# Kernel optimization log

Hardware: AMD Instinct MI355X
Metric: run time of the kernel (lower is better)

## Reference

```python
import jax, jax.numpy as jnp
import numpy as np

D_MODEL = 1024
HEADS = 16
D_K = D_MODEL // HEADS
B, S = 2, 2048


def setup_inputs() -> dict:
    key = jax.random.key(0)
    ks = jax.random.split(key, 11)
    sc = 1.0 / np.sqrt(D_MODEL)
    return {
        "q": jax.random.normal(ks[0], (B, S, D_MODEL), jnp.float32),
        "k": jax.random.normal(ks[1], (B, S, D_MODEL), jnp.float32),
        "v": jax.random.normal(ks[2], (B, S, D_MODEL), jnp.float32),
        "Wq": jax.random.normal(ks[3], (D_MODEL, D_MODEL), jnp.float32) * sc,
        "bq": jnp.zeros((D_MODEL,), jnp.float32),
        "Wk": jax.random.normal(ks[4], (D_MODEL, D_MODEL), jnp.float32) * sc,
        "bk": jnp.zeros((D_MODEL,), jnp.float32),
        "Wv": jax.random.normal(ks[5], (D_MODEL, D_MODEL), jnp.float32) * sc,
        "bv": jnp.zeros((D_MODEL,), jnp.float32),
        "Wo": jax.random.normal(ks[6], (D_MODEL, D_MODEL), jnp.float32) * sc,
        "bo": jnp.zeros((D_MODEL,), jnp.float32),
    }


def reference(q, k, v, Wq, bq, Wk, bk, Wv, bv, Wo, bo):
    bs = q.shape[0]
    # linear projections then split heads: [B,S,D] -> [B,H,S,Dk]
    def proj(x, W, b):
        y = x @ W.T + b
        return y.reshape(bs, -1, HEADS, D_K).transpose(0, 2, 1, 3)

    qh = proj(q, Wq, bq)
    kh = proj(k, Wk, bk)
    vh = proj(v, Wv, bv)
    # scores: [B,H,Sq,Sk] -- full attention matrix as in the original
    scores = jnp.einsum("bhqd,bhkd->bhqk", qh, kh) / jnp.sqrt(
        jnp.asarray(D_K, jnp.float32))
    attn = jax.nn.softmax(scores, axis=-1)
    # dropout is identity in eval/reference mode
    out = jnp.einsum("bhqk,bhkd->bhqd", attn, vh)
    concat = out.transpose(0, 2, 1, 3).reshape(bs, -1, D_MODEL)
    return concat @ Wo.T + bo
```

## Files before the change

kernel.cpp:

```cpp
#include <hip/hip_runtime.h>
#include <hip/hip_bf16.h>

typedef __attribute__((ext_vector_type(8))) short bf16x8;
typedef __attribute__((ext_vector_type(4))) float f32x4;
typedef __attribute__((ext_vector_type(16))) float f32x16;

#define DM   1024
#define SEQ  2048
#define NB   2
#define NH   16
#define MR   (NB*SEQ)

#define SMK  (MR*DM)
#define W1M  (DM*DM)

#define QSCALE 0.18033688011112042f

#define OFF_QB  ((size_t)0)
#define OFF_KB  ((size_t)SMK)
#define OFF_VB  ((size_t)(2*(size_t)SMK))
#define OFF_WQ  ((size_t)(3*(size_t)SMK))
#define OFF_WO  ((size_t)(3*(size_t)SMK + 3*(size_t)W1M))
#define OFF_QP  ((size_t)(3*(size_t)SMK + 4*(size_t)W1M))
#define OFF_KP  ((size_t)(4*(size_t)SMK + 4*(size_t)W1M))
#define OFF_VP  ((size_t)(5*(size_t)SMK + 4*(size_t)W1M))
#define OFF_CC  ((size_t)0)

__device__ __forceinline__ unsigned short f2bf(float f) {
  union { __hip_bfloat16 b; unsigned short u; } cv;
  cv.b = __float2bfloat16(f);
  return cv.u;
}

__device__ __forceinline__ unsigned int cvtpk_bf16(float lo, float hi) {
  unsigned int r;
  asm("v_cvt_pk_bf16_f32 %0, %1, %2" : "=v"(r) : "v"(lo), "v"(hi));
  return r;
}

__device__ __forceinline__ void plane32_swap(unsigned int& a, unsigned int& b) {
  asm("v_permlane32_swap_b32 %0, %1" : "+v"(a), "+v"(b));
}

__global__ __launch_bounds__(256) void cvt_inputs(const float* __restrict__ q,
                                                  const float* __restrict__ k,
                                                  const float* __restrict__ v,
                                                  unsigned short* __restrict__ dst) {
  const int z = blockIdx.y;
  const float* src = (z == 0) ? q : ((z == 1) ? k : v);
  int i = blockIdx.x * 256 + threadIdx.x;
  float4 val = reinterpret_cast<const float4*>(src)[i];
  ushort4 o;
  o.x = f2bf(val.x); o.y = f2bf(val.y); o.z = f2bf(val.z); o.w = f2bf(val.w);
  reinterpret_cast<ushort4*>(dst + (size_t)z * SMK)[i] = o;
}

__global__ __launch_bounds__(256) void cvt_weights(const float* __restrict__ wq,
                                                   const float* __restrict__ wk,
                                                   const float* __restrict__ wv,
                                                   const float* __restrict__ wo,
                                                   unsigned short* __restrict__ dst) {
  const int z = blockIdx.y;
  const float* src = (z == 0) ? wq : ((z == 1) ? wk : ((z == 2) ? wv : wo));
  int i = blockIdx.x * 256 + threadIdx.x;
  float4 val = reinterpret_cast<const float4*>(src)[i];
  ushort4 o;
  o.x = f2bf(val.x); o.y = f2bf(val.y); o.z = f2bf(val.z); o.w = f2bf(val.w);
  reinterpret_cast<ushort4*>(dst + (size_t)z * W1M)[i] = o;
}

__device__ __forceinline__ void gload_lds16(const void* g, void* l) {
  __builtin_amdgcn_global_load_lds(
      (const __attribute__((address_space(1))) unsigned int*)g,
      (__attribute__((address_space(3))) unsigned int*)l,
      16, 0, 0);
}

template<int BM, int BN, bool OUT_BF16, bool BIAS_ROW>
__device__ __forceinline__ void gemm_bt_body(unsigned short* __restrict__ As,
                                             unsigned short* __restrict__ Bs,
                                             const unsigned short* __restrict__ A,
                                             const unsigned short* __restrict__ Bt,
                                             const float* __restrict__ bias,
                                             void* __restrict__ Cv,
                                             int N, int K, float scale,
                                             int brow, int bcol) {
  constexpr int MREP = BM / 32;
  constexpr int NREP = BN / 32;
  const int tid  = threadIdx.x;
  const int lane = tid & 63;
  const int w    = tid >> 6;
  const int wr   = w >> 1, wc = w & 1;

  f32x4 acc[MREP][NREP];
#pragma unroll
  for (int m = 0; m < MREP; m++)
#pragma unroll
    for (int n = 0; n < NREP; n++) acc[m][n] = (f32x4){0.f, 0.f, 0.f, 0.f};

  const int srow = lane >> 2;
  const int scol = (lane & 3) * 8;

  auto stage = [&](int buf, int k0) {
#pragma unroll
    for (int c = w; c < BM / 16; c += 4)
      gload_lds16(A + (size_t)(brow + c * 16 + srow) * K + k0 + scol,
                  (char*)As + (size_t)buf * BM * 64 + c * 1024);
#pragma unroll
    for (int c = w; c < BN / 16; c += 4)
      gload_lds16(Bt + (size_t)(bcol + c * 16 + srow) * K + k0 + scol,
                  (char*)Bs + (size_t)buf * BN * 64 + c * 1024);
  };

  stage(0, 0);
  __syncthreads();

  const int nk = K / 32;
  const int lrow_a = wr * (BM / 2) + (lane & 15);
  const int lrow_b = wc * (BN / 2) + (lane & 15);
  const int lcol   = (lane >> 4) * 8;

  for (int kt = 0; kt < nk; ++kt) {
    int buf = kt & 1;
    if (kt + 1 < nk) stage(buf ^ 1, (kt + 1) * 32);
    bf16x8 a[MREP], b[NREP];
#pragma unroll
    for (int m = 0; m < MREP; m++)
      a[m] = *(const bf16x8*)&As[(size_t)buf * BM * 32 + (lrow_a + m * 16) * 32 + lcol];
#pragma unroll
    for (int n = 0; n < NREP; n++)
      b[n] = *(const bf16x8*)&Bs[(size_t)buf * BN * 32 + (lrow_b + n * 16) * 32 + lcol];
    __builtin_amdgcn_s_setprio(1);
#pragma unroll
    for (int m = 0; m < MREP; m++)
#pragma unroll
      for (int n = 0; n < NREP; n++)
        acc[m][n] = __builtin_amdgcn_mfma_f32_16x16x32_bf16(a[m], b[n], acc[m][n], 0, 0, 0);
    __builtin_amdgcn_s_setprio(0);
    __syncthreads();
  }

  const int crow0 = brow + wr * (BM / 2);
  const int ccol0 = bcol + wc * (BN / 2);
  const int rsub  = (lane >> 4) * 4;
  const int csub  = lane & 15;
#pragma unroll
  for (int m = 0; m < MREP; m++)
#pragma unroll
    for (int n = 0; n < NREP; n++) {
      int col = ccol0 + n * 16 + csub;
      float bcol_v = BIAS_ROW ? 0.f : bias[col];
#pragma unroll
      for (int q = 0; q < 4; q++) {
        int row = crow0 + m * 16 + rsub + q;
        float bb = BIAS_ROW ? bias[row] : bcol_v;
        float v = (acc[m][n][q] + bb) * scale;
        if (OUT_BF16)
          ((unsigned short*)Cv)[(size_t)row * N + col] = f2bf(v);
        else
          ((float*)Cv)[(size_t)row * N + col] = v;
      }
    }
}

__global__ __launch_bounds__(256) void gemm_qkv(unsigned short* ws,
                                                const float* __restrict__ bq,
                                                const float* __restrict__ bk,
                                                const float* __restrict__ bv) {
  __shared__ unsigned short As[2 * 128 * 32];
  __shared__ unsigned short Bs[2 * 128 * 32];
  const int z = blockIdx.z;
  const int bid = blockIdx.x;
  if (z < 2) {
    int bx = bid & 7, by = bid >> 3;
    gemm_bt_body<128, 128, true, false>(
        As, Bs,
        ws + OFF_QB + (size_t)z * SMK, ws + OFF_WQ + (size_t)z * W1M,
        z ? bk : bq, ws + OFF_QP + (size_t)z * SMK,
        DM, DM, z ? 1.f : QSCALE, by * 128, bx * 128);
  } else {
    int bx = bid & 31, by = bid >> 5;
    gemm_bt_body<128, 128, true, true>(
        As, Bs,
        ws + OFF_WQ + 2 * W1M, ws + OFF_VB,
        bv, ws + OFF_VP,
        MR, DM, 1.f, by * 128, bx * 128);
  }
}

__global__ __launch_bounds__(256) void gemm_out(const unsigned short* __restrict__ ws,
                                                const float* __restrict__ bo,
                                                float* __restrict__ out) {
  __shared__ unsigned short As[2 * 64 * 32];
  __shared__ unsigned short Bs[2 * 128 * 32];
  gemm_bt_body<64, 128, false, false>(
      As, Bs,
      ws + OFF_CC, ws + OFF_WO, bo, out,
      DM, DM, 1.f, blockIdx.y * 64, blockIdx.x * 128);
}

__global__ __launch_bounds__(512, 4) void flash_attn(unsigned short* ws) {
  __shared__ __align__(16) unsigned char smem[65536];

  const int tid  = threadIdx.x;
  const int lane = tid & 63;
  const int w    = tid >> 6;
  const int s    = w >> 2;
  const int wsub = w & 3;
  const int q    = lane & 31;
  const int hi   = lane >> 5;
  const int swq  = q & 7;
  const int bid  = blockIdx.x;
  const int swzb = (bid & 7) * 64 + (bid >> 3);
  const int qblk = swzb & 15;
  const int bh   = swzb >> 4;
  const int b    = bh >> 4, h = bh & 15;

  const unsigned short* Qp = ws + OFF_QP;
  const unsigned short* Kp = ws + OFF_KP;
  const unsigned short* Vp = ws + OFF_VP;
  unsigned short* CC = ws + OFF_CC;

  const unsigned short* Kg = Kp + (size_t)(b * SEQ) * DM + h * 64;
  const unsigned short* Vg = Vp + (size_t)(h * 64) * MR + (size_t)b * SEQ;

  bf16x8 bqf[4];
  {
    const unsigned short* qrow =
        Qp + (size_t)(b * SEQ + qblk * 128 + wsub * 32 + q) * DM + h * 64;
#pragma unroll
    for (int c = 0; c < 4; c++)
      bqf[c] = *(const bf16x8*)(qrow + c * 16 + hi * 8);
  }

  f32x16 o_acc[2];
#pragma unroll
  for (int dt = 0; dt < 2; dt++)
#pragma unroll
    for (int r = 0; r < 16; r++) o_acc[dt][r] = 0.f;
  float l_run = 0.f;

  auto stage = [&](int buf, int t) {
    const unsigned short* Kt = Kg + (size_t)(s * 16 + t) * 64 * DM;
    const unsigned short* Vt = Vg + (s * 16 + t) * 64;
    char* base = (char*)smem + (size_t)(s * 2 + buf) * 16384;
#pragma unroll
    for (int i = 0; i < 2; i++) {
      int slot = wsub * 128 + i * 64 + lane;
      int srow = slot >> 3;
      int gch  = (slot & 7) ^ (srow & 7);
      gload_lds16(Kt + (size_t)srow * DM + gch * 8, base + slot * 16);
      gload_lds16(Vt + (size_t)srow * MR + gch * 8, base + 8192 + slot * 16);
    }
  };

  stage(0, 0);

  for (int t = 0; t < 16; ++t) {
    int buf = t & 1;
    __syncthreads();
    if (t + 1 < 16) stage(buf ^ 1, t + 1);
    const unsigned short* Kb = (const unsigned short*)(smem + (size_t)(s * 2 + buf) * 16384);
    const unsigned short* Vb = Kb + 4096;

    f32x16 st0, st1;
#pragma unroll
    for (int r = 0; r < 16; r++) { st0[r] = 0.f; st1[r] = 0.f; }
    __builtin_amdgcn_s_setprio(1);
#pragma unroll
    for (int c = 0; c < 4; c++) {
      int ch = (((c << 1) | hi) ^ swq) << 3;
      bf16x8 ak0 = *(const bf16x8*)&Kb[q * 64 + ch];
      bf16x8 ak1 = *(const bf16x8*)&Kb[(32 + q) * 64 + ch];
      st0 = __builtin_amdgcn_mfma_f32_32x32x16_bf16(ak0, bqf[c], st0, 0, 0, 0);
      st1 = __builtin_amdgcn_mfma_f32_32x32x16_bf16(ak1, bqf[c], st1, 0, 0, 0);
    }
    __builtin_amdgcn_s_setprio(0);

    unsigned int pk0[8], pk1[8];
    float lt = 0.f;
#pragma unroll
    for (int p = 0; p < 8; p++) {
      float a0 = __builtin_amdgcn_exp2f(st0[2 * p]);
      float a1 = __builtin_amdgcn_exp2f(st0[2 * p + 1]);
      float b0 = __builtin_amdgcn_exp2f(st1[2 * p]);
      float b1 = __builtin_amdgcn_exp2f(st1[2 * p + 1]);
      lt += (a0 + a1) + (b0 + b1);
      pk0[p] = cvtpk_bf16(a0, a1);
      pk1[p] = cvtpk_bf16(b0, b1);
    }
    l_run += lt;

    plane32_swap(pk0[0], pk0[2]); plane32_swap(pk0[1], pk0[3]);
    plane32_swap(pk0[4], pk0[6]); plane32_swap(pk0[5], pk0[7]);
    plane32_swap(pk1[0], pk1[2]); plane32_swap(pk1[1], pk1[3]);
    plane32_swap(pk1[4], pk1[6]); plane32_swap(pk1[5], pk1[7]);

    __builtin_amdgcn_s_setprio(1);
#pragma unroll
    for (int t4 = 0; t4 < 4; t4++) {
      union { unsigned int u[4]; bf16x8 v; } pb;
      const unsigned int* src = (t4 < 2) ? pk0 : pk1;
      pb.u[0] = src[(t4 & 1) * 4 + 0];
      pb.u[1] = src[(t4 & 1) * 4 + 1];
      pb.u[2] = src[(t4 & 1) * 4 + 2];
      pb.u[3] = src[(t4 & 1) * 4 + 3];
      int ch = (((t4 << 1) | hi) ^ swq) << 3;
#pragma unroll
      for (int dt = 0; dt < 2; dt++) {
        bf16x8 av = *(const bf16x8*)&Vb[(dt * 32 + q) * 64 + ch];
        o_acc[dt] = __builtin_amdgcn_mfma_f32_32x32x16_bf16(av, pb.v, o_acc[dt], 0, 0, 0);
      }
    }
    __builtin_amdgcn_s_setprio(0);
  }

  __syncthreads();
  float* scr = (float*)smem;
  float lsum = l_run + __shfl_xor(l_run, 32, 64);
  if (s == 1) {
    int idx = (wsub * 64 + lane) * 33;
#pragma unroll
    for (int dt = 0; dt < 2; dt++)
#pragma unroll
      for (int r = 0; r < 16; r++) scr[idx + dt * 16 + r] = o_acc[dt][r];
    scr[idx + 32] = lsum;
  }
  __syncthreads();
  if (s == 0) {
    int idx = (wsub * 64 + lane) * 33;
#pragma unroll
    for (int dt = 0; dt < 2; dt++)
#pragma unroll
      for (int r = 0; r < 16; r++) o_acc[dt][r] += scr[idx + dt * 16 + r];
    float l = lsum + scr[idx + 32];
    float inv = 1.f / l;

    int qg = b * SEQ + qblk * 128 + wsub * 32 + q;
    unsigned short* crow = CC + (size_t)qg * DM + h * 64;
#pragma unroll
    for (int dt = 0; dt < 2; dt++)
#pragma unroll
      for (int rq = 0; rq < 4; rq++) {
        ushort4 o;
        o.x = f2bf(o_acc[dt][4 * rq + 0] * inv);
        o.y = f2bf(o_acc[dt][4 * rq + 1] * inv);
        o.z = f2bf(o_acc[dt][4 * rq + 2] * inv);
        o.w = f2bf(o_acc[dt][4 * rq + 3] * inv);
        *(ushort4*)&crow[dt * 32 + rq * 8 + hi * 4] = o;
      }
  }
}

extern "C" void kernel_launch(void* const* d_in, const int* in_sizes, int n_in,
                              void* d_out, int out_size, void* d_ws, size_t ws_size,
                              hipStream_t stream) {
  const float* q  = (const float*)d_in[0];
  const float* k  = (const float*)d_in[1];
  const float* v  = (const float*)d_in[2];
  const float* Wq = (const float*)d_in[3];
  const float* bq = (const float*)d_in[4];
  const float* Wk = (const float*)d_in[5];
  const float* bk = (const float*)d_in[6];
  const float* Wv = (const float*)d_in[7];
  const float* bv = (const float*)d_in[8];
  const float* Wo = (const float*)d_in[9];
  const float* bo = (const float*)d_in[10];

  unsigned short* ws = (unsigned short*)d_ws;
  float* out = (float*)d_out;

  cvt_inputs<<<dim3(SMK / 1024, 3), dim3(256), 0, stream>>>(q, k, v, ws + OFF_QB);
  cvt_weights<<<dim3(W1M / 1024, 4), dim3(256), 0, stream>>>(Wq, Wk, Wv, Wo, ws + OFF_WQ);

  gemm_qkv<<<dim3(256, 1, 3), dim3(256), 0, stream>>>(ws, bq, bk, bv);

  flash_attn<<<dim3(512), dim3(512), 0, stream>>>(ws);

  gemm_out<<<dim3(DM / 128, MR / 64, 1), dim3(256), 0, stream>>>(ws, bo, out);
}
```

Before: 126.0 us.

## Triple-buffer GEMM and attention loads, double query rows per attention block

```diff
diff --git a/kernel.cpp b/kernel.cpp
--- a/kernel.cpp
+++ b/kernel.cpp
@@ -87,6 +87,7 @@
                                              int brow, int bcol) {
   constexpr int MREP = BM / 32;
   constexpr int NREP = BN / 32;
+  constexpr int LPS  = BM / 64 + BN / 64;
   const int tid  = threadIdx.x;
   const int lane = tid & 63;
   const int w    = tid >> 6;
@@ -113,23 +114,34 @@
   };
 
   stage(0, 0);
-  __syncthreads();
+  stage(1, 32);
 
   const int nk = K / 32;
   const int lrow_a = wr * (BM / 2) + (lane & 15);
   const int lrow_b = wc * (BN / 2) + (lane & 15);
   const int lcol   = (lane >> 4) * 8;
 
+  int b0 = 0;
   for (int kt = 0; kt < nk; ++kt) {
-    int buf = kt & 1;
-    if (kt + 1 < nk) stage(buf ^ 1, (kt + 1) * 32);
+    if (kt + 1 < nk) {
+      if constexpr (LPS == 4) asm volatile("s_waitcnt vmcnt(4)" ::: "memory");
+      else                    asm volatile("s_waitcnt vmcnt(3)" ::: "memory");
+    } else {
+      asm volatile("s_waitcnt vmcnt(0)" ::: "memory");
+    }
+    __builtin_amdgcn_s_barrier();
+    __builtin_amdgcn_sched_barrier(0);
+    if (kt + 2 < nk) {
+      int bn = b0 + 2; if (bn >= 3) bn -= 3;
+      stage(bn, (kt + 2) * 32);
+    }
     bf16x8 a[MREP], b[NREP];
 #pragma unroll
     for (int m = 0; m < MREP; m++)
-      a[m] = *(const bf16x8*)&As[(size_t)buf * BM * 32 + (lrow_a + m * 16) * 32 + lcol];
+      a[m] = *(const bf16x8*)&As[(size_t)b0 * BM * 32 + (lrow_a + m * 16) * 32 + lcol];
 #pragma unroll
     for (int n = 0; n < NREP; n++)
-      b[n] = *(const bf16x8*)&Bs[(size_t)buf * BN * 32 + (lrow_b + n * 16) * 32 + lcol];
+      b[n] = *(const bf16x8*)&Bs[(size_t)b0 * BN * 32 + (lrow_b + n * 16) * 32 + lcol];
     __builtin_amdgcn_s_setprio(1);
 #pragma unroll
     for (int m = 0; m < MREP; m++)
@@ -137,7 +149,7 @@
       for (int n = 0; n < NREP; n++)
         acc[m][n] = __builtin_amdgcn_mfma_f32_16x16x32_bf16(a[m], b[n], acc[m][n], 0, 0, 0);
     __builtin_amdgcn_s_setprio(0);
-    __syncthreads();
+    b0 = (b0 == 2) ? 0 : b0 + 1;
   }
 
   const int crow0 = brow + wr * (BM / 2);
@@ -151,10 +163,10 @@
       int col = ccol0 + n * 16 + csub;
       float bcol_v = BIAS_ROW ? 0.f : bias[col];
 #pragma unroll
-      for (int q = 0; q < 4; q++) {
-        int row = crow0 + m * 16 + rsub + q;
+      for (int qq = 0; qq < 4; qq++) {
+        int row = crow0 + m * 16 + rsub + qq;
         float bb = BIAS_ROW ? bias[row] : bcol_v;
-        float v = (acc[m][n][q] + bb) * scale;
+        float v = (acc[m][n][qq] + bb) * scale;
         if (OUT_BF16)
           ((unsigned short*)Cv)[(size_t)row * N + col] = f2bf(v);
         else
@@ -167,8 +179,8 @@
                                                 const float* __restrict__ bq,
                                                 const float* __restrict__ bk,
                                                 const float* __restrict__ bv) {
-  __shared__ unsigned short As[2 * 128 * 32];
-  __shared__ unsigned short Bs[2 * 128 * 32];
+  __shared__ unsigned short As[3 * 128 * 32];
+  __shared__ unsigned short Bs[3 * 128 * 32];
   const int z = blockIdx.z;
   const int bid = blockIdx.x;
   if (z < 2) {
@@ -191,16 +203,16 @@
 __global__ __launch_bounds__(256) void gemm_out(const unsigned short* __restrict__ ws,
                                                 const float* __restrict__ bo,
                                                 float* __restrict__ out) {
-  __shared__ unsigned short As[2 * 64 * 32];
-  __shared__ unsigned short Bs[2 * 128 * 32];
+  __shared__ unsigned short As[3 * 64 * 32];
+  __shared__ unsigned short Bs[3 * 128 * 32];
   gemm_bt_body<64, 128, false, false>(
       As, Bs,
       ws + OFF_CC, ws + OFF_WO, bo, out,
       DM, DM, 1.f, blockIdx.y * 64, blockIdx.x * 128);
 }
 
-__global__ __launch_bounds__(512, 4) void flash_attn(unsigned short* ws) {
-  __shared__ __align__(16) unsigned char smem[65536];
+__global__ __launch_bounds__(512, 2) void flash_attn(unsigned short* ws) {
+  __shared__ __align__(16) unsigned char smem[98304];
 
   const int tid  = threadIdx.x;
   const int lane = tid & 63;
@@ -211,9 +223,9 @@
   const int hi   = lane >> 5;
   const int swq  = q & 7;
   const int bid  = blockIdx.x;
-  const int swzb = (bid & 7) * 64 + (bid >> 3);
-  const int qblk = swzb & 15;
-  const int bh   = swzb >> 4;
+  const int swzb = (bid & 7) * 32 + (bid >> 3);
+  const int qblk = swzb & 7;
+  const int bh   = swzb >> 3;
   const int b    = bh >> 4, h = bh & 15;
 
   const unsigned short* Qp = ws + OFF_QP;
@@ -224,26 +236,29 @@
   const unsigned short* Kg = Kp + (size_t)(b * SEQ) * DM + h * 64;
   const unsigned short* Vg = Vp + (size_t)(h * 64) * MR + (size_t)b * SEQ;
 
-  bf16x8 bqf[4];
-  {
+  bf16x8 bqf[2][4];
+#pragma unroll
+  for (int s2 = 0; s2 < 2; s2++) {
     const unsigned short* qrow =
-        Qp + (size_t)(b * SEQ + qblk * 128 + wsub * 32 + q) * DM + h * 64;
+        Qp + (size_t)(b * SEQ + qblk * 256 + wsub * 64 + s2 * 32 + q) * DM + h * 64;
 #pragma unroll
     for (int c = 0; c < 4; c++)
-      bqf[c] = *(const bf16x8*)(qrow + c * 16 + hi * 8);
-  }
-
-  f32x16 o_acc[2];
-#pragma unroll
-  for (int dt = 0; dt < 2; dt++)
-#pragma unroll
-    for (int r = 0; r < 16; r++) o_acc[dt][r] = 0.f;
-  float l_run = 0.f;
+      bqf[s2][c] = *(const bf16x8*)(qrow + c * 16 + hi * 8);
+  }
+
+  f32x16 o_acc[2][2];
+  float l_run[2] = {0.f, 0.f};
+#pragma unroll
+  for (int s2 = 0; s2 < 2; s2++)
+#pragma unroll
+    for (int dt = 0; dt < 2; dt++)
+#pragma unroll
+      for (int r = 0; r < 16; r++) o_acc[s2][dt][r] = 0.f;
 
   auto stage = [&](int buf, int t) {
     const unsigned short* Kt = Kg + (size_t)(s * 16 + t) * 64 * DM;
     const unsigned short* Vt = Vg + (s * 16 + t) * 64;
-    char* base = (char*)smem + (size_t)(s * 2 + buf) * 16384;
+    char* base = (char*)smem + (size_t)(s * 3 + buf) * 16384;
 #pragma unroll
     for (int i = 0; i < 2; i++) {
       int slot = wsub * 128 + i * 64 + lane;
@@ -255,100 +270,125 @@
   };
 
   stage(0, 0);
-
+  stage(1, 1);
+
+  int bcur = 0;
   for (int t = 0; t < 16; ++t) {
-    int buf = t & 1;
-    __syncthreads();
-    if (t + 1 < 16) stage(buf ^ 1, t + 1);
-    const unsigned short* Kb = (const unsigned short*)(smem + (size_t)(s * 2 + buf) * 16384);
+    if (t < 15) asm volatile("s_waitcnt vmcnt(4)" ::: "memory");
+    else        asm volatile("s_waitcnt vmcnt(0)" ::: "memory");
+    __builtin_amdgcn_s_barrier();
+    __builtin_amdgcn_sched_barrier(0);
+    if (t + 2 < 16) {
+      int bn = bcur + 2; if (bn >= 3) bn -= 3;
+      stage(bn, t + 2);
+    }
+    const unsigned short* Kb = (const unsigned short*)(smem + (size_t)(s * 3 + bcur) * 16384);
     const unsigned short* Vb = Kb + 4096;
 
-    f32x16 st0, st1;
-#pragma unroll
-    for (int r = 0; r < 16; r++) { st0[r] = 0.f; st1[r] = 0.f; }
+    f32x16 st[2][2];
+#pragma unroll
+    for (int s2 = 0; s2 < 2; s2++)
+#pragma unroll
+      for (int r = 0; r < 16; r++) { st[s2][0][r] = 0.f; st[s2][1][r] = 0.f; }
     __builtin_amdgcn_s_setprio(1);
 #pragma unroll
     for (int c = 0; c < 4; c++) {
       int ch = (((c << 1) | hi) ^ swq) << 3;
       bf16x8 ak0 = *(const bf16x8*)&Kb[q * 64 + ch];
       bf16x8 ak1 = *(const bf16x8*)&Kb[(32 + q) * 64 + ch];
-      st0 = __builtin_amdgcn_mfma_f32_32x32x16_bf16(ak0, bqf[c], st0, 0, 0, 0);
-      st1 = __builtin_amdgcn_mfma_f32_32x32x16_bf16(ak1, bqf[c], st1, 0, 0, 0);
+      st[0][0] = __builtin_amdgcn_mfma_f32_32x32x16_bf16(ak0, bqf[0][c], st[0][0], 0, 0, 0);
+      st[0][1] = __builtin_amdgcn_mfma_f32_32x32x16_bf16(ak1, bqf[0][c], st[0][1], 0, 0, 0);
+      st[1][0] = __builtin_amdgcn_mfma_f32_32x32x16_bf16(ak0, bqf[1][c], st[1][0], 0, 0, 0);
+      st[1][1] = __builtin_amdgcn_mfma_f32_32x32x16_bf16(ak1, bqf[1][c], st[1][1], 0, 0, 0);
     }
     __builtin_amdgcn_s_setprio(0);
 
-    unsigned int pk0[8], pk1[8];
-    float lt = 0.f;
-#pragma unroll
-    for (int p = 0; p < 8; p++) {
-      float a0 = __builtin_amdgcn_exp2f(st0[2 * p]);
-      float a1 = __builtin_amdgcn_exp2f(st0[2 * p + 1]);
-      float b0 = __builtin_amdgcn_exp2f(st1[2 * p]);
-      float b1 = __builtin_amdgcn_exp2f(st1[2 * p + 1]);
-      lt += (a0 + a1) + (b0 + b1);
-      pk0[p] = cvtpk_bf16(a0, a1);
-      pk1[p] = cvtpk_bf16(b0, b1);
-    }
-    l_run += lt;
-
-    plane32_swap(pk0[0], pk0[2]); plane32_swap(pk0[1], pk0[3]);
-    plane32_swap(pk0[4], pk0[6]); plane32_swap(pk0[5], pk0[7]);
-    plane32_swap(pk1[0], pk1[2]); plane32_swap(pk1[1], pk1[3]);
-    plane32_swap(pk1[4], pk1[6]); plane32_swap(pk1[5], pk1[7]);
+    unsigned int pk[2][2][8];
+#pragma unroll
+    for (int s2 = 0; s2 < 2; s2++) {
+      float lt = 0.f;
+#pragma unroll
+      for (int p = 0; p < 8; p++) {
+        float e0 = __builtin_amdgcn_exp2f(st[s2][0][2 * p]);
+        float e1 = __builtin_amdgcn_exp2f(st[s2][0][2 * p + 1]);
+        float e2 = __builtin_amdgcn_exp2f(st[s2][1][2 * p]);
+        float e3 = __builtin_amdgcn_exp2f(st[s2][1][2 * p + 1]);
+        lt += (e0 + e1) + (e2 + e3);
+        pk[s2][0][p] = cvtpk_bf16(e0, e1);
+        pk[s2][1][p] = cvtpk_bf16(e2, e3);
+      }
+      l_run[s2] += lt;
+      plane32_swap(pk[s2][0][0], pk[s2][0][2]); plane32_swap(pk[s2][0][1], pk[s2][0][3]);
+      plane32_swap(pk[s2][0][4], pk[s2][0][6]); plane32_swap(pk[s2][0][5], pk[s2][0][7]);
+      plane32_swap(pk[s2][1][0], pk[s2][1][2]); plane32_swap(pk[s2][1][1], pk[s2][1][3]);
+      plane32_swap(pk[s2][1][4], pk[s2][1][6]); plane32_swap(pk[s2][1][5], pk[s2][1][7]);
+    }
 
     __builtin_amdgcn_s_setprio(1);
 #pragma unroll
     for (int t4 = 0; t4 < 4; t4++) {
-      union { unsigned int u[4]; bf16x8 v; } pb;
-      const unsigned int* src = (t4 < 2) ? pk0 : pk1;
-      pb.u[0] = src[(t4 & 1) * 4 + 0];
-      pb.u[1] = src[(t4 & 1) * 4 + 1];
-      pb.u[2] = src[(t4 & 1) * 4 + 2];
-      pb.u[3] = src[(t4 & 1) * 4 + 3];
       int ch = (((t4 << 1) | hi) ^ swq) << 3;
+      union { unsigned int u[4]; bf16x8 v; } pb0, pb1;
+#pragma unroll
+      for (int j = 0; j < 4; j++) {
+        pb0.u[j] = pk[0][t4 >> 1][(t4 & 1) * 4 + j];
+        pb1.u[j] = pk[1][t4 >> 1][(t4 & 1) * 4 + j];
+      }
 #pragma unroll
       for (int dt = 0; dt < 2; dt++) {
         bf16x8 av = *(const bf16x8*)&Vb[(dt * 32 + q) * 64 + ch];
-        o_acc[dt] = __builtin_amdgcn_mfma_f32_32x32x16_bf16(av, pb.v, o_acc[dt], 0, 0, 0);
+        o_acc[0][dt] = __builtin_amdgcn_mfma_f32_32x32x16_bf16(av, pb0.v, o_acc[0][dt], 0, 0, 0);
+        o_acc[1][dt] = __builtin_amdgcn_mfma_f32_32x32x16_bf16(av, pb1.v, o_acc[1][dt], 0, 0, 0);
       }
     }
     __builtin_amdgcn_s_setprio(0);
+    bcur = (bcur == 2) ? 0 : bcur + 1;
   }
 
   __syncthreads();
   float* scr = (float*)smem;
-  float lsum = l_run + __shfl_xor(l_run, 32, 64);
+  float lsum[2];
+#pragma unroll
+  for (int s2 = 0; s2 < 2; s2++)
+    lsum[s2] = l_run[s2] + __shfl_xor(l_run[s2], 32, 64);
+  const int gi = wsub * 64 + lane;
   if (s == 1) {
-    int idx = (wsub * 64 + lane) * 33;
-#pragma unroll
-    for (int dt = 0; dt < 2; dt++)
-#pragma unroll
-      for (int r = 0; r < 16; r++) scr[idx + dt * 16 + r] = o_acc[dt][r];
-    scr[idx + 32] = lsum;
+#pragma unroll
+    for (int s2 = 0; s2 < 2; s2++) {
+#pragma unroll
+      for (int dt = 0; dt < 2; dt++)
+#pragma unroll
+        for (int r = 0; r < 16; r++)
+          scr[gi * 67 + s2 * 33 + dt * 16 + r] = o_acc[s2][dt][r];
+      scr[gi * 67 + s2 * 33 + 32] = lsum[s2];
+    }
   }
   __syncthreads();
   if (s == 0) {
-    int idx = (wsub * 64 + lane) * 33;
-#pragma unroll
-    for (int dt = 0; dt < 2; dt++)
-#pragma unroll
-      for (int r = 0; r < 16; r++) o_acc[dt][r] += scr[idx + dt * 16 + r];
-    float l = lsum + scr[idx + 32];
-    float inv = 1.f / l;
-
-    int qg = b * SEQ + qblk * 128 + wsub * 32 + q;
-    unsigned short* crow = CC + (size_t)qg * DM + h * 64;
-#pragma unroll
-    for (int dt = 0; dt < 2; dt++)
-#pragma unroll
-      for (int rq = 0; rq < 4; rq++) {
-        ushort4 o;
-        o.x = f2bf(o_acc[dt][4 * rq + 0] * inv);
-        o.y = f2bf(o_acc[dt][4 * rq + 1] * inv);
-        o.z = f2bf(o_acc[dt][4 * rq + 2] * inv);
-        o.w = f2bf(o_acc[dt][4 * rq + 3] * inv);
-        *(ushort4*)&crow[dt * 32 + rq * 8 + hi * 4] = o;
-      }
+#pragma unroll
+    for (int s2 = 0; s2 < 2; s2++) {
+#pragma unroll
+      for (int dt = 0; dt < 2; dt++)
+#pragma unroll
+        for (int r = 0; r < 16; r++)
+          o_acc[s2][dt][r] += scr[gi * 67 + s2 * 33 + dt * 16 + r];
+      float l = lsum[s2] + scr[gi * 67 + s2 * 33 + 32];
+      float inv = 1.f / l;
+
+      int qg = b * SEQ + qblk * 256 + wsub * 64 + s2 * 32 + q;
+      unsigned short* crow = CC + (size_t)qg * DM + h * 64;
+#pragma unroll
+      for (int dt = 0; dt < 2; dt++)
+#pragma unroll
+        for (int rq = 0; rq < 4; rq++) {
+          ushort4 o;
+          o.x = f2bf(o_acc[s2][dt][4 * rq + 0] * inv);
+          o.y = f2bf(o_acc[s2][dt][4 * rq + 1] * inv);
+          o.z = f2bf(o_acc[s2][dt][4 * rq + 2] * inv);
+          o.w = f2bf(o_acc[s2][dt][4 * rq + 3] * inv);
+          *(ushort4*)&crow[dt * 32 + rq * 8 + hi * 4] = o;
+        }
+    }
   }
 }
 
@@ -375,7 +415,7 @@
 
   gemm_qkv<<<dim3(256, 1, 3), dim3(256), 0, stream>>>(ws, bq, bk, bv);
 
-  flash_attn<<<dim3(512), dim3(512), 0, stream>>>(ws);
+  flash_attn<<<dim3(256), dim3(512), 0, stream>>>(ws);
 
   gemm_out<<<dim3(DM / 128, MR / 64, 1), dim3(256), 0, stream>>>(ws, bo, out);
 }
```

Result: faster. 120.9 us (-4.0%).

## Triple-buffer GEMM LDS staging with vmcnt waits and merge conversion kernels

Applied to the files above, without the earlier changes.

```diff
diff --git a/kernel.cpp b/kernel.cpp
--- a/kernel.cpp
+++ b/kernel.cpp
@@ -42,31 +42,34 @@
   asm("v_permlane32_swap_b32 %0, %1" : "+v"(a), "+v"(b));
 }
 
-__global__ __launch_bounds__(256) void cvt_inputs(const float* __restrict__ q,
-                                                  const float* __restrict__ k,
-                                                  const float* __restrict__ v,
-                                                  unsigned short* __restrict__ dst) {
-  const int z = blockIdx.y;
-  const float* src = (z == 0) ? q : ((z == 1) ? k : v);
+__global__ __launch_bounds__(256) void cvt_all(const float* __restrict__ q,
+                                               const float* __restrict__ k,
+                                               const float* __restrict__ v,
+                                               const float* __restrict__ wq,
+                                               const float* __restrict__ wk,
+                                               const float* __restrict__ wv,
+                                               const float* __restrict__ wo,
+                                               unsigned short* __restrict__ ws) {
   int i = blockIdx.x * 256 + threadIdx.x;
-  float4 val = reinterpret_cast<const float4*>(src)[i];
+  const float* src;
+  unsigned short* dst;
+  int j;
+  if (i < 3 * (SMK / 4)) {
+    int z = i >> 20;
+    j = i & ((SMK / 4) - 1);
+    src = (z == 0) ? q : ((z == 1) ? k : v);
+    dst = ws + OFF_QB + (size_t)z * SMK;
+  } else {
+    int i2 = i - 3 * (SMK / 4);
+    int z = i2 >> 18;
+    j = i2 & ((W1M / 4) - 1);
+    src = (z == 0) ? wq : ((z == 1) ? wk : ((z == 2) ? wv : wo));
+    dst = ws + OFF_WQ + (size_t)z * W1M;
+  }
+  float4 val = reinterpret_cast<const float4*>(src)[j];
   ushort4 o;
   o.x = f2bf(val.x); o.y = f2bf(val.y); o.z = f2bf(val.z); o.w = f2bf(val.w);
-  reinterpret_cast<ushort4*>(dst + (size_t)z * SMK)[i] = o;
-}
-
-__global__ __launch_bounds__(256) void cvt_weights(const float* __restrict__ wq,
-                                                   const float* __restrict__ wk,
-                                                   const float* __restrict__ wv,
-                                                   const float* __restrict__ wo,
-                                                   unsigned short* __restrict__ dst) {
-  const int z = blockIdx.y;
-  const float* src = (z == 0) ? wq : ((z == 1) ? wk : ((z == 2) ? wv : wo));
-  int i = blockIdx.x * 256 + threadIdx.x;
-  float4 val = reinterpret_cast<const float4*>(src)[i];
-  ushort4 o;
-  o.x = f2bf(val.x); o.y = f2bf(val.y); o.z = f2bf(val.z); o.w = f2bf(val.w);
-  reinterpret_cast<ushort4*>(dst + (size_t)z * W1M)[i] = o;
+  reinterpret_cast<ushort4*>(dst)[j] = o;
 }
 
 __device__ __forceinline__ void gload_lds16(const void* g, void* l) {
@@ -87,6 +90,7 @@
                                              int brow, int bcol) {
   constexpr int MREP = BM / 32;
   constexpr int NREP = BN / 32;
+  constexpr int LPS  = BM / 64 + BN / 64;
   const int tid  = threadIdx.x;
   const int lane = tid & 63;
   const int w    = tid >> 6;
@@ -113,23 +117,34 @@
   };
 
   stage(0, 0);
-  __syncthreads();
+  stage(1, 32);
 
   const int nk = K / 32;
   const int lrow_a = wr * (BM / 2) + (lane & 15);
   const int lrow_b = wc * (BN / 2) + (lane & 15);
   const int lcol   = (lane >> 4) * 8;
 
+  int b0 = 0;
   for (int kt = 0; kt < nk; ++kt) {
-    int buf = kt & 1;
-    if (kt + 1 < nk) stage(buf ^ 1, (kt + 1) * 32);
+    if (kt + 1 < nk) {
+      if constexpr (LPS == 4) asm volatile("s_waitcnt vmcnt(4)" ::: "memory");
+      else                    asm volatile("s_waitcnt vmcnt(3)" ::: "memory");
+    } else {
+      asm volatile("s_waitcnt vmcnt(0)" ::: "memory");
+    }
+    __builtin_amdgcn_s_barrier();
+    __builtin_amdgcn_sched_barrier(0);
+    if (kt + 2 < nk) {
+      int bn = b0 + 2; if (bn >= 3) bn -= 3;
+      stage(bn, (kt + 2) * 32);
+    }
     bf16x8 a[MREP], b[NREP];
 #pragma unroll
     for (int m = 0; m < MREP; m++)
-      a[m] = *(const bf16x8*)&As[(size_t)buf * BM * 32 + (lrow_a + m * 16) * 32 + lcol];
+      a[m] = *(const bf16x8*)&As[(size_t)b0 * BM * 32 + (lrow_a + m * 16) * 32 + lcol];
 #pragma unroll
     for (int n = 0; n < NREP; n++)
-      b[n] = *(const bf16x8*)&Bs[(size_t)buf * BN * 32 + (lrow_b + n * 16) * 32 + lcol];
+      b[n] = *(const bf16x8*)&Bs[(size_t)b0 * BN * 32 + (lrow_b + n * 16) * 32 + lcol];
     __builtin_amdgcn_s_setprio(1);
 #pragma unroll
     for (int m = 0; m < MREP; m++)
@@ -137,7 +152,7 @@
       for (int n = 0; n < NREP; n++)
         acc[m][n] = __builtin_amdgcn_mfma_f32_16x16x32_bf16(a[m], b[n], acc[m][n], 0, 0, 0);
     __builtin_amdgcn_s_setprio(0);
-    __syncthreads();
+    b0 = (b0 == 2) ? 0 : b0 + 1;
   }
 
   const int crow0 = brow + wr * (BM / 2);
@@ -151,10 +166,10 @@
       int col = ccol0 + n * 16 + csub;
       float bcol_v = BIAS_ROW ? 0.f : bias[col];
 #pragma unroll
-      for (int q = 0; q < 4; q++) {
-        int row = crow0 + m * 16 + rsub + q;
+      for (int qq = 0; qq < 4; qq++) {
+        int row = crow0 + m * 16 + rsub + qq;
         float bb = BIAS_ROW ? bias[row] : bcol_v;
-        float v = (acc[m][n][q] + bb) * scale;
+        float v = (acc[m][n][qq] + bb) * scale;
         if (OUT_BF16)
           ((unsigned short*)Cv)[(size_t)row * N + col] = f2bf(v);
         else
@@ -167,8 +182,8 @@
                                                 const float* __restrict__ bq,
                                                 const float* __restrict__ bk,
                                                 const float* __restrict__ bv) {
-  __shared__ unsigned short As[2 * 128 * 32];
-  __shared__ unsigned short Bs[2 * 128 * 32];
+  __shared__ unsigned short As[3 * 128 * 32];
+  __shared__ unsigned short Bs[3 * 128 * 32];
   const int z = blockIdx.z;
   const int bid = blockIdx.x;
   if (z < 2) {
@@ -191,8 +206,8 @@
 __global__ __launch_bounds__(256) void gemm_out(const unsigned short* __restrict__ ws,
                                                 const float* __restrict__ bo,
                                                 float* __restrict__ out) {
-  __shared__ unsigned short As[2 * 64 * 32];
-  __shared__ unsigned short Bs[2 * 128 * 32];
+  __shared__ unsigned short As[3 * 64 * 32];
+  __shared__ unsigned short Bs[3 * 128 * 32];
   gemm_bt_body<64, 128, false, false>(
       As, Bs,
       ws + OFF_CC, ws + OFF_WO, bo, out,
@@ -370,8 +385,8 @@
   unsigned short* ws = (unsigned short*)d_ws;
   float* out = (float*)d_out;
 
-  cvt_inputs<<<dim3(SMK / 1024, 3), dim3(256), 0, stream>>>(q, k, v, ws + OFF_QB);
-  cvt_weights<<<dim3(W1M / 1024, 4), dim3(256), 0, stream>>>(Wq, Wk, Wv, Wo, ws + OFF_WQ);
+  cvt_all<<<dim3((3 * (SMK / 4) + 4 * (W1M / 4)) / 256), dim3(256), 0, stream>>>(
+      q, k, v, Wq, Wk, Wv, Wo, ws);
 
   gemm_qkv<<<dim3(256, 1, 3), dim3(256), 0, stream>>>(ws, bq, bk, bv);
 
```

Result: faster. 121.1 us (-3.9%).
